# Optimization experiments

Measured on AMD Instinct MI355X. Metric: run time of the kernel, lower is better.

## Reference

```python
import jax, jax.numpy as jnp
import numpy as np

D = 11           # num_classes + 1 (embedding dim)
HL = 7           # window height = 1 + 2*H_PAD
WL = 7           # window width  = 1 + 2*W_PAD
PAD = 3
MAXH, MAXW = 30, 30
FF = 64          # dim_feedforward
EPS = 1e-5       # LayerNorm eps (torch default)
PAD_VALUE = 0.0


def setup_inputs() -> dict:
    key = jax.random.key(0)
    ks = jax.random.split(key, 6)
    N, C, H, W = 1, 10, 16, 16
    s = 0.1
    return {
        "x": jax.random.uniform(ks[0], (N, C, H, W), jnp.float32),
        "Wqkv": jax.random.normal(ks[1], (3 * D, D), jnp.float32) * s,  # in_proj_weight
        "Wo": jax.random.normal(ks[2], (D, D), jnp.float32) * s,        # out_proj.weight
        "W1": jax.random.normal(ks[3], (FF, D), jnp.float32) * s,       # linear1.weight
        "W2": jax.random.normal(ks[4], (D, FF), jnp.float32) * s,       # linear2.weight
        "ln1_w": jnp.ones((D,), jnp.float32),                           # norm1.weight (bias=False)
        "ln2_w": jnp.ones((D,), jnp.float32),                           # norm2.weight (bias=False)
    }


def _layer_norm(x, w):
    m = jnp.mean(x, axis=-1, keepdims=True)
    v = jnp.mean(jnp.square(x - m), axis=-1, keepdims=True)
    return (x - m) / jnp.sqrt(v + EPS) * w


def _encoder_layer(x, Wqkv, Wo, W1, W2, ln1_w, ln2_w):
    # x: [B, S, D]; post-norm, 1 head, no biases, eval mode (dropout off)
    qkv = x @ Wqkv.T
    q, k, v = jnp.split(qkv, 3, axis=-1)
    scale = 1.0 / jnp.sqrt(jnp.float32(D))
    attn = jax.nn.softmax(jnp.einsum('bqd,bkd->bqk', q, k) * scale, axis=-1)
    sa = jnp.einsum('bqk,bkd->bqd', attn, v) @ Wo.T
    x = _layer_norm(x + sa, ln1_w)
    ff = jax.nn.relu(x @ W1.T) @ W2.T
    return _layer_norm(x + ff, ln2_w)


def reference(x, Wqkv, Wo, W1, W2, ln1_w, ln2_w):
    N, C, H, W = x.shape
    C1 = C + 1
    # mask channel: 1 in the padded border, 0 inside
    mask = jnp.pad(jnp.zeros((N, 1, H, W), x.dtype),
                   ((0, 0), (0, 0), (PAD, PAD), (PAD, PAD)), constant_values=1.0)
    xp = jnp.pad(x, ((0, 0), (0, 0), (PAD, PAD), (PAD, PAD)), constant_values=PAD_VALUE)
    xp = jnp.concatenate([xp, mask], axis=1)            # [N, C+1, H+6, W+6]
    win = jnp.stack([xp[:, :, i:i + H, j:j + W]
                     for i in range(HL) for j in range(WL)], axis=-1)  # [N, C1, H, W, 49]
    win = jnp.transpose(win, (0, 2, 3, 1, 4))           # [N, H, W, C1, 49]
    win = win.reshape(N * H * W * C1, HL, WL)
    # embed window into max_height x max_width canvas (rest = pad_value)
    canvas = jnp.full((N * H * W * C1, MAXH, MAXW), PAD_VALUE, x.dtype)
    canvas = canvas.at[:, :HL, :WL].set(win)
    seq = canvas.reshape(N * H * W, C1, MAXH * MAXW).transpose(0, 2, 1)  # [B, S=900, D=11]
    out = _encoder_layer(seq, Wqkv, Wo, W1, W2, ln1_w, ln2_w)
    return out.transpose(0, 2, 1)[:, :-1]               # [B, C, 900]
```

## Files before the change

kernel.cpp:

```cpp
#include <hip/hip_runtime.h>


#define D 11
#define ROWP 12
#define NW 49
#define NWP 52
#define NR 50
#define SEQ 900
#define FFD 64
#define CIN 10
#define NB 256
#define TPB 576
#define NRD (NR * D)

__device__ __forceinline__ float dot12(const float4* a, const float4* b) {
    float4 s = make_float4(0.f, 0.f, 0.f, 0.f);
    #pragma unroll
    for (int i = 0; i < 3; ++i) {
        float4 x = a[i], y = b[i];
        s.x += x.x * y.x; s.y += x.y * y.y; s.z += x.z * y.z; s.w += x.w * y.w;
    }
    return s.x + s.y + s.z + s.w;
}

__global__ __launch_bounds__(TPB) void pve_kernel(
    const float* __restrict__ gx,
    const float* __restrict__ gWqkv,
    const float* __restrict__ gWo,
    const float* __restrict__ gW1,
    const float* __restrict__ gW2,
    const float* __restrict__ gln1,
    const float* __restrict__ gln2,
    float* __restrict__ out)
{
    __shared__ __align__(16) float sQ[33 * ROWP];
    __shared__ __align__(16) float sWo[D * ROWP];
    __shared__ __align__(16) float sW1[FFD * ROWP];
    __shared__ __align__(16) float sW2[D * FFD];
    __shared__ float sln1[D], sln2[D];
    __shared__ __align__(16) float sSeq[NR][ROWP];
    __shared__ __align__(16) float sK[NW][ROWP];
    __shared__ __align__(16) float sVt[D][NWP];
    __shared__ __align__(16) float sQr[NR][ROWP];
    __shared__ __align__(16) float sE[NR][NWP];
    __shared__ __align__(16) float sNum[NR][ROWP];
    __shared__ float sDen[NR];
    __shared__ __align__(16) float sX1[NR][ROWP];
    __shared__ __align__(16) float sX1n[NR][ROWP];
    __shared__ __align__(16) float sH[NR][FFD];
    __shared__ __align__(16) float sY[NR][ROWP];
    __shared__ __align__(16) float sR[NR][ROWP];

    const int tid = threadIdx.x;
    const int b = blockIdx.x;
    const int h = b >> 4;
    const int w = b & 15;

    const int rd = tid;
    const int r = rd / D;
    const int d = rd - r * D;

    for (int i = tid; i < 33 * ROWP; i += TPB) {
        const int rr = i / ROWP, cc = i - rr * ROWP;
        sQ[i] = (cc < D) ? gWqkv[rr * D + cc] : 0.f;
    }
    for (int i = tid; i < D * ROWP; i += TPB) {
        const int rr = i / ROWP, cc = i - rr * ROWP;
        sWo[i] = (cc < D) ? gWo[rr * D + cc] : 0.f;
    }
    for (int i = tid; i < FFD * ROWP; i += TPB) {
        const int rr = i / ROWP, cc = i - rr * ROWP;
        sW1[i] = (cc < D) ? gW1[rr * D + cc] : 0.f;
    }
    for (int i = tid; i < D * FFD; i += TPB) sW2[i] = gW2[i];
    if (tid < D) { sln1[tid] = gln1[tid]; sln2[tid] = gln2[tid]; }

    if (rd < NRD) {
        float val = 0.0f;
        if (r < NW) {
            const int i = r / 7, j = r - (r / 7) * 7;
            const int y = h + i, xx = w + j;
            const bool inter = (y >= 3) && (y < 19) && (xx >= 3) && (xx < 19);
            const int base = inter ? ((y - 3) * 16 + (xx - 3)) : 0;
            if (d < CIN) val = inter ? gx[d * 256 + base] : 0.0f;
            else         val = inter ? 0.0f : 1.0f;
        }
        sSeq[r][d] = val;
        if (d == CIN) sSeq[r][D] = 0.f;
    }
    __syncthreads();

    if (rd < NRD) {
        const float4* sv = (const float4*)&sSeq[r][0];
        const float aq = dot12(sv, (const float4*)&sQ[d * ROWP]);
        const float ak = dot12(sv, (const float4*)&sQ[(D + d) * ROWP]);
        const float av = dot12(sv, (const float4*)&sQ[(2 * D + d) * ROWP]);
        sQr[r][d] = aq;
        if (d == CIN) sQr[r][D] = 0.f;
        if (r < NW) { sK[r][d] = ak; sVt[d][r] = av;
                      if (d == CIN) sK[r][D] = 0.f; }
        else { sVt[d][NW] = 0.f; sVt[d][NW + 1] = 0.f; sVt[d][NW + 2] = 0.f; }
    }
    __syncthreads();

    {
        const float scale = 0.30151134457776363f;
        #pragma unroll
        for (int k = 0; k < 5; ++k) {
            const int idx = tid + k * TPB;
            if (idx < NR * NWP) {
                const int rr = idx / NWP;
                const int tt = idx - rr * NWP;
                float e = 0.f;
                if (tt < NW) {
                    const float s = dot12((const float4*)&sQr[rr][0],
                                          (const float4*)&sK[tt][0]);
                    e = __expf(s * scale);
                }
                sE[rr][tt] = e;
            }
        }
    }
    __syncthreads();

    if (rd < NRD) {
        const float4* ev = (const float4*)&sE[r][0];
        const float4* vv = (const float4*)&sVt[d][0];
        float4 an = make_float4(0.f, 0.f, 0.f, 0.f);
        float4 ad = make_float4(0.f, 0.f, 0.f, 0.f);
        #pragma unroll
        for (int i = 0; i < 13; ++i) {
            const float4 e = ev[i], v = vv[i];
            an.x += e.x * v.x; an.y += e.y * v.y;
            an.z += e.z * v.z; an.w += e.w * v.w;
            ad.x += e.x; ad.y += e.y; ad.z += e.z; ad.w += e.w;
        }
        sNum[r][d] = an.x + an.y + an.z + an.w;
        if (d == CIN) sNum[r][D] = 0.f;
        if (d == 0) sDen[r] = 851.0f + ad.x + ad.y + ad.z + ad.w;
    }
    __syncthreads();

    if (rd < NRD) {
        const float acc = dot12((const float4*)&sNum[r][0],
                                (const float4*)&sWo[d * ROWP]);
        sX1[r][d] = sSeq[r][d] + acc / sDen[r];
        if (d == CIN) sX1[r][D] = 0.f;
    }
    __syncthreads();

    if (rd < NRD) {
        const float4* xv = (const float4*)&sX1[r][0];
        float4 s4 = make_float4(0.f, 0.f, 0.f, 0.f);
        float4 q4 = make_float4(0.f, 0.f, 0.f, 0.f);
        #pragma unroll
        for (int i = 0; i < 3; ++i) {
            const float4 x = xv[i];
            s4.x += x.x; s4.y += x.y; s4.z += x.z; s4.w += x.w;
            q4.x += x.x * x.x; q4.y += x.y * x.y;
            q4.z += x.z * x.z; q4.w += x.w * x.w;
        }
        const float sum = s4.x + s4.y + s4.z + s4.w;
        const float sq  = q4.x + q4.y + q4.z + q4.w;
        const float m   = sum * (1.0f / 11.0f);
        const float var = sq * (1.0f / 11.0f) - m * m;
        sX1n[r][d] = (sX1[r][d] - m) * rsqrtf(var + 1e-5f) * sln1[d];
        if (d == CIN) sX1n[r][D] = 0.f;
    }
    __syncthreads();

    #pragma unroll
    for (int k = 0; k < 6; ++k) {
        const int idx = tid + k * TPB;
        if (idx < NR * FFD) {
            const int rr = idx >> 6;
            const int ff = idx & 63;
            const float acc = dot12((const float4*)&sX1n[rr][0],
                                    (const float4*)&sW1[ff * ROWP]);
            sH[rr][ff] = fmaxf(acc, 0.0f);
        }
    }
    __syncthreads();

    if (rd < NRD) {
        const float4* hv = (const float4*)&sH[r][0];
        const float4* wv = (const float4*)&sW2[d * FFD];
        float4 a4 = make_float4(0.f, 0.f, 0.f, 0.f);
        #pragma unroll
        for (int i = 0; i < 16; ++i) {
            const float4 hh = hv[i], ww = wv[i];
            a4.x += hh.x * ww.x; a4.y += hh.y * ww.y;
            a4.z += hh.z * ww.z; a4.w += hh.w * ww.w;
        }
        sY[r][d] = sX1n[r][d] + a4.x + a4.y + a4.z + a4.w;
        if (d == CIN) sY[r][D] = 0.f;
    }
    __syncthreads();

    if (rd < NRD) {
        const float4* yv = (const float4*)&sY[r][0];
        float4 s4 = make_float4(0.f, 0.f, 0.f, 0.f);
        float4 q4 = make_float4(0.f, 0.f, 0.f, 0.f);
        #pragma unroll
        for (int i = 0; i < 3; ++i) {
            const float4 y = yv[i];
            s4.x += y.x; s4.y += y.y; s4.z += y.z; s4.w += y.w;
            q4.x += y.x * y.x; q4.y += y.y * y.y;
            q4.z += y.z * y.z; q4.w += y.w * y.w;
        }
        const float sum = s4.x + s4.y + s4.z + s4.w;
        const float sq  = q4.x + q4.y + q4.z + q4.w;
        const float m   = sum * (1.0f / 11.0f);
        const float var = sq * (1.0f / 11.0f) - m * m;
        sR[r][d] = (sY[r][d] - m) * rsqrtf(var + 1e-5f) * sln2[d];
    }
    __syncthreads();

    float4* ob4 = (float4*)(out + b * (CIN * SEQ));
    #pragma unroll
    for (int k = 0; k < 4; ++k) {
        const int qi = tid + k * TPB;
        if (qi < 2250) {
            const int c  = qi / 225;
            const int s0 = (qi - c * 225) * 4;
            float4 v4;
            float* pv = (float*)&v4;
            #pragma unroll
            for (int u = 0; u < 4; ++u) {
                const int s = s0 + u;
                const int i = s / 30;
                const int j = s - i * 30;
                pv[u] = (i < 7 && j < 7) ? sR[i * 7 + j][c] : sR[NW][c];
            }
            ob4[qi] = v4;
        }
    }
}

extern "C" void kernel_launch(void* const* d_in, const int* in_sizes, int n_in,
                              void* d_out, int out_size, void* d_ws, size_t ws_size,
                              hipStream_t stream) {
    (void)in_sizes; (void)n_in; (void)out_size; (void)d_ws; (void)ws_size;
    const float* x    = (const float*)d_in[0];
    const float* Wqkv = (const float*)d_in[1];
    const float* Wo   = (const float*)d_in[2];
    const float* W1   = (const float*)d_in[3];
    const float* W2   = (const float*)d_in[4];
    const float* ln1  = (const float*)d_in[5];
    const float* ln2  = (const float*)d_in[6];
    pve_kernel<<<NB, TPB, 0, stream>>>(x, Wqkv, Wo, W1, W2, ln1, ln2,
                                       (float*)d_out);
}
```

Before: 79.80 us.

## Map 16 lanes per row and replace block barriers with wave-local syncs and shuffles

Reassigns threads so each sequence row owns a 16-lane group, with 832 threads per block. This keeps every per-row stage (softmax denominator, attention numerator, both LayerNorms, FFN) inside one wavefront, so several __syncthreads become wave barriers and the row reductions use xor shuffles instead of shared-memory round trips. Several intermediate shared buffers are dropped and the W2 and H rows are padded. The trade-off is more idle lanes (5 of 16 per row) and a larger block, and correctness now depends on each row never crossing a wave boundary.

```diff
diff --git a/kernel.cpp b/kernel.cpp
--- a/kernel.cpp
+++ b/kernel.cpp
@@ -4,14 +4,15 @@
 #define D 11
 #define ROWP 12
 #define NW 49
+#define NR 50
 #define NWP 52
-#define NR 50
+#define FFD 64
+#define W2P 68
+#define HP  68
+#define CIN 10
 #define SEQ 900
-#define FFD 64
-#define CIN 10
 #define NB 256
-#define TPB 576
-#define NRD (NR * D)
+#define TPB 832
 
 __device__ __forceinline__ float dot12(const float4* a, const float4* b) {
     float4 s = make_float4(0.f, 0.f, 0.f, 0.f);
@@ -21,6 +22,12 @@
         s.x += x.x * y.x; s.y += x.y * y.y; s.z += x.z * y.z; s.w += x.w * y.w;
     }
     return s.x + s.y + s.z + s.w;
+}
+
+__device__ __forceinline__ void wave_sync() {
+    __builtin_amdgcn_wave_barrier();
+    asm volatile("s_waitcnt lgkmcnt(0)" ::: "memory");
+    __builtin_amdgcn_wave_barrier();
 }
 
 __global__ __launch_bounds__(TPB) void pve_kernel(
@@ -36,19 +43,15 @@
     __shared__ __align__(16) float sQ[33 * ROWP];
     __shared__ __align__(16) float sWo[D * ROWP];
     __shared__ __align__(16) float sW1[FFD * ROWP];
-    __shared__ __align__(16) float sW2[D * FFD];
-    __shared__ float sln1[D], sln2[D];
+    __shared__ __align__(16) float sW2[D * W2P];
     __shared__ __align__(16) float sSeq[NR][ROWP];
     __shared__ __align__(16) float sK[NW][ROWP];
     __shared__ __align__(16) float sVt[D][NWP];
     __shared__ __align__(16) float sQr[NR][ROWP];
     __shared__ __align__(16) float sE[NR][NWP];
     __shared__ __align__(16) float sNum[NR][ROWP];
-    __shared__ float sDen[NR];
-    __shared__ __align__(16) float sX1[NR][ROWP];
     __shared__ __align__(16) float sX1n[NR][ROWP];
-    __shared__ __align__(16) float sH[NR][FFD];
-    __shared__ __align__(16) float sY[NR][ROWP];
+    __shared__ __align__(16) float sH[NR][HP];
     __shared__ __align__(16) float sR[NR][ROWP];
 
     const int tid = threadIdx.x;
@@ -56,9 +59,10 @@
     const int h = b >> 4;
     const int w = b & 15;
 
-    const int rd = tid;
-    const int r = rd / D;
-    const int d = rd - r * D;
+    const int r = tid >> 4;
+    const int d = tid & 15;
+    const bool rowv = (r < NR);
+    const bool dv = (d < D);
 
     for (int i = tid; i < 33 * ROWP; i += TPB) {
         const int rr = i / ROWP, cc = i - rr * ROWP;
@@ -72,119 +76,140 @@
         const int rr = i / ROWP, cc = i - rr * ROWP;
         sW1[i] = (cc < D) ? gW1[rr * D + cc] : 0.f;
     }
-    for (int i = tid; i < D * FFD; i += TPB) sW2[i] = gW2[i];
-    if (tid < D) { sln1[tid] = gln1[tid]; sln2[tid] = gln2[tid]; }
-
-    if (rd < NRD) {
-        float val = 0.0f;
-        if (r < NW) {
-            const int i = r / 7, j = r - (r / 7) * 7;
-            const int y = h + i, xx = w + j;
-            const bool inter = (y >= 3) && (y < 19) && (xx >= 3) && (xx < 19);
-            const int base = inter ? ((y - 3) * 16 + (xx - 3)) : 0;
-            if (d < CIN) val = inter ? gx[d * 256 + base] : 0.0f;
-            else         val = inter ? 0.0f : 1.0f;
-        }
-        sSeq[r][d] = val;
-        if (d == CIN) sSeq[r][D] = 0.f;
+    for (int i = tid; i < D * W2P; i += TPB) {
+        const int rr = i / W2P, cc = i - rr * W2P;
+        sW2[i] = (cc < FFD) ? gW2[rr * FFD + cc] : 0.f;
+    }
+    float lnw1 = 0.f, lnw2 = 0.f;
+    if (dv) { lnw1 = gln1[d]; lnw2 = gln2[d]; }
+
+    float xin = 0.f;
+    if (rowv) {
+        if (dv) {
+            if (r < NW) {
+                const int i7 = r / 7, j7 = r - i7 * 7;
+                const int y = h + i7, xx = w + j7;
+                const bool inter = (y >= 3) && (y < 19) && (xx >= 3) && (xx < 19);
+                const int base = inter ? ((y - 3) * 16 + (xx - 3)) : 0;
+                if (d < CIN) xin = inter ? gx[d * 256 + base] : 0.0f;
+                else         xin = inter ? 0.0f : 1.0f;
+            }
+            sSeq[r][d] = xin;
+        } else if (d == D) {
+            sSeq[r][D] = 0.f;
+        }
     }
     __syncthreads();
 
-    if (rd < NRD) {
-        const float4* sv = (const float4*)&sSeq[r][0];
-        const float aq = dot12(sv, (const float4*)&sQ[d * ROWP]);
-        const float ak = dot12(sv, (const float4*)&sQ[(D + d) * ROWP]);
-        const float av = dot12(sv, (const float4*)&sQ[(2 * D + d) * ROWP]);
-        sQr[r][d] = aq;
-        if (d == CIN) sQr[r][D] = 0.f;
-        if (r < NW) { sK[r][d] = ak; sVt[d][r] = av;
-                      if (d == CIN) sK[r][D] = 0.f; }
-        else { sVt[d][NW] = 0.f; sVt[d][NW + 1] = 0.f; sVt[d][NW + 2] = 0.f; }
+    if (rowv) {
+        if (dv) {
+            const float4* sv = (const float4*)&sSeq[r][0];
+            const float aq = dot12(sv, (const float4*)&sQ[d * ROWP]);
+            const float ak = dot12(sv, (const float4*)&sQ[(D + d) * ROWP]);
+            const float av = dot12(sv, (const float4*)&sQ[(2 * D + d) * ROWP]);
+            sQr[r][d] = aq;
+            if (r < NW) { sK[r][d] = ak; sVt[d][r] = av; }
+            else { sVt[d][NW] = 0.f; sVt[d][NW + 1] = 0.f; sVt[d][NW + 2] = 0.f; }
+        } else if (d == D) {
+            sQr[r][D] = 0.f;
+            if (r < NW) sK[r][D] = 0.f;
+        }
     }
     __syncthreads();
 
-    {
+    float den = 851.0f;
+    if (rowv) {
         const float scale = 0.30151134457776363f;
+        const float4* qv = (const float4*)&sQr[r][0];
+        const float4 q0 = qv[0], q1 = qv[1], q2 = qv[2];
+        float psum = 0.f;
         #pragma unroll
-        for (int k = 0; k < 5; ++k) {
-            const int idx = tid + k * TPB;
-            if (idx < NR * NWP) {
-                const int rr = idx / NWP;
-                const int tt = idx - rr * NWP;
+        for (int it = 0; it < 4; ++it) {
+            const int tt = d + (it << 4);
+            if (tt < NWP) {
                 float e = 0.f;
                 if (tt < NW) {
-                    const float s = dot12((const float4*)&sQr[rr][0],
-                                          (const float4*)&sK[tt][0]);
+                    const float4* kv = (const float4*)&sK[tt][0];
+                    const float4 k0 = kv[0], k1 = kv[1], k2 = kv[2];
+                    const float s =
+                        q0.x*k0.x + q0.y*k0.y + q0.z*k0.z + q0.w*k0.w +
+                        q1.x*k1.x + q1.y*k1.y + q1.z*k1.z + q1.w*k1.w +
+                        q2.x*k2.x + q2.y*k2.y + q2.z*k2.z + q2.w*k2.w;
                     e = __expf(s * scale);
                 }
-                sE[rr][tt] = e;
-            }
-        }
-    }
-    __syncthreads();
-
-    if (rd < NRD) {
-        const float4* ev = (const float4*)&sE[r][0];
-        const float4* vv = (const float4*)&sVt[d][0];
-        float4 an = make_float4(0.f, 0.f, 0.f, 0.f);
-        float4 ad = make_float4(0.f, 0.f, 0.f, 0.f);
-        #pragma unroll
-        for (int i = 0; i < 13; ++i) {
-            const float4 e = ev[i], v = vv[i];
-            an.x += e.x * v.x; an.y += e.y * v.y;
-            an.z += e.z * v.z; an.w += e.w * v.w;
-            ad.x += e.x; ad.y += e.y; ad.z += e.z; ad.w += e.w;
-        }
-        sNum[r][d] = an.x + an.y + an.z + an.w;
-        if (d == CIN) sNum[r][D] = 0.f;
-        if (d == 0) sDen[r] = 851.0f + ad.x + ad.y + ad.z + ad.w;
-    }
-    __syncthreads();
-
-    if (rd < NRD) {
+                sE[r][tt] = e;
+                psum += e;
+            }
+        }
+        psum += __shfl_xor(psum, 8, 16);
+        psum += __shfl_xor(psum, 4, 16);
+        psum += __shfl_xor(psum, 2, 16);
+        psum += __shfl_xor(psum, 1, 16);
+        den += psum;
+    }
+    wave_sync();
+
+    if (rowv) {
+        if (dv) {
+            const float4* ev = (const float4*)&sE[r][0];
+            const float4* vv = (const float4*)&sVt[d][0];
+            float4 an = make_float4(0.f, 0.f, 0.f, 0.f);
+            #pragma unroll
+            for (int i = 0; i < 13; ++i) {
+                const float4 e = ev[i], v = vv[i];
+                an.x += e.x * v.x; an.y += e.y * v.y;
+                an.z += e.z * v.z; an.w += e.w * v.w;
+            }
+            sNum[r][d] = an.x + an.y + an.z + an.w;
+        } else if (d == D) {
+            sNum[r][D] = 0.f;
+        }
+    }
+    wave_sync();
+
+    float x1 = 0.f;
+    if (rowv && dv) {
         const float acc = dot12((const float4*)&sNum[r][0],
                                 (const float4*)&sWo[d * ROWP]);
-        sX1[r][d] = sSeq[r][d] + acc / sDen[r];
-        if (d == CIN) sX1[r][D] = 0.f;
-    }
-    __syncthreads();
-
-    if (rd < NRD) {
-        const float4* xv = (const float4*)&sX1[r][0];
-        float4 s4 = make_float4(0.f, 0.f, 0.f, 0.f);
-        float4 q4 = make_float4(0.f, 0.f, 0.f, 0.f);
+        x1 = xin + acc / den;
+    }
+    {
+        float s1 = x1, s2 = x1 * x1;
+        s1 += __shfl_xor(s1, 8, 16); s2 += __shfl_xor(s2, 8, 16);
+        s1 += __shfl_xor(s1, 4, 16); s2 += __shfl_xor(s2, 4, 16);
+        s1 += __shfl_xor(s1, 2, 16); s2 += __shfl_xor(s2, 2, 16);
+        s1 += __shfl_xor(s1, 1, 16); s2 += __shfl_xor(s2, 1, 16);
+        const float m   = s1 * (1.0f / 11.0f);
+        const float var = s2 * (1.0f / 11.0f) - m * m;
+        x1 = (x1 - m) * rsqrtf(var + 1e-5f) * lnw1;
+    }
+    if (rowv) {
+        if (dv) sX1n[r][d] = x1;
+        else if (d == D) sX1n[r][D] = 0.f;
+    }
+    wave_sync();
+
+    if (rowv) {
+        const float4* xv = (const float4*)&sX1n[r][0];
+        const float4 xa = xv[0], xb = xv[1], xc = xv[2];
         #pragma unroll
-        for (int i = 0; i < 3; ++i) {
-            const float4 x = xv[i];
-            s4.x += x.x; s4.y += x.y; s4.z += x.z; s4.w += x.w;
-            q4.x += x.x * x.x; q4.y += x.y * x.y;
-            q4.z += x.z * x.z; q4.w += x.w * x.w;
-        }
-        const float sum = s4.x + s4.y + s4.z + s4.w;
-        const float sq  = q4.x + q4.y + q4.z + q4.w;
-        const float m   = sum * (1.0f / 11.0f);
-        const float var = sq * (1.0f / 11.0f) - m * m;
-        sX1n[r][d] = (sX1[r][d] - m) * rsqrtf(var + 1e-5f) * sln1[d];
-        if (d == CIN) sX1n[r][D] = 0.f;
-    }
-    __syncthreads();
-
-    #pragma unroll
-    for (int k = 0; k < 6; ++k) {
-        const int idx = tid + k * TPB;
-        if (idx < NR * FFD) {
-            const int rr = idx >> 6;
-            const int ff = idx & 63;
-            const float acc = dot12((const float4*)&sX1n[rr][0],
-                                    (const float4*)&sW1[ff * ROWP]);
-            sH[rr][ff] = fmaxf(acc, 0.0f);
-        }
-    }
-    __syncthreads();
-
-    if (rd < NRD) {
+        for (int it = 0; it < 4; ++it) {
+            const int ff = d + (it << 4);
+            const float4* wv = (const float4*)&sW1[ff * ROWP];
+            const float4 w0 = wv[0], w1 = wv[1], w2 = wv[2];
+            const float acc =
+                xa.x*w0.x + xa.y*w0.y + xa.z*w0.z + xa.w*w0.w +
+                xb.x*w1.x + xb.y*w1.y + xb.z*w1.z + xb.w*w1.w +
+                xc.x*w2.x + xc.y*w2.y + xc.z*w2.z + xc.w*w2.w;
+            sH[r][ff] = fmaxf(acc, 0.0f);
+        }
+    }
+    wave_sync();
+
+    float yv = 0.f;
+    if (rowv && dv) {
         const float4* hv = (const float4*)&sH[r][0];
-        const float4* wv = (const float4*)&sW2[d * FFD];
+        const float4* wv = (const float4*)&sW2[d * W2P];
         float4 a4 = make_float4(0.f, 0.f, 0.f, 0.f);
         #pragma unroll
         for (int i = 0; i < 16; ++i) {
@@ -192,33 +217,23 @@
             a4.x += hh.x * ww.x; a4.y += hh.y * ww.y;
             a4.z += hh.z * ww.z; a4.w += hh.w * ww.w;
         }
-        sY[r][d] = sX1n[r][d] + a4.x + a4.y + a4.z + a4.w;
-        if (d == CIN) sY[r][D] = 0.f;
-    }
-    __syncthreads();
-
-    if (rd < NRD) {
-        const float4* yv = (const float4*)&sY[r][0];
-        float4 s4 = make_float4(0.f, 0.f, 0.f, 0.f);
-        float4 q4 = make_float4(0.f, 0.f, 0.f, 0.f);
-        #pragma unroll
-        for (int i = 0; i < 3; ++i) {
-            const float4 y = yv[i];
-            s4.x += y.x; s4.y += y.y; s4.z += y.z; s4.w += y.w;
-            q4.x += y.x * y.x; q4.y += y.y * y.y;
-            q4.z += y.z * y.z; q4.w += y.w * y.w;
-        }
-        const float sum = s4.x + s4.y + s4.z + s4.w;
-        const float sq  = q4.x + q4.y + q4.z + q4.w;
-        const float m   = sum * (1.0f / 11.0f);
-        const float var = sq * (1.0f / 11.0f) - m * m;
-        sR[r][d] = (sY[r][d] - m) * rsqrtf(var + 1e-5f) * sln2[d];
+        yv = x1 + a4.x + a4.y + a4.z + a4.w;
+    }
+    {
+        float s1 = yv, s2 = yv * yv;
+        s1 += __shfl_xor(s1, 8, 16); s2 += __shfl_xor(s2, 8, 16);
+        s1 += __shfl_xor(s1, 4, 16); s2 += __shfl_xor(s2, 4, 16);
+        s1 += __shfl_xor(s1, 2, 16); s2 += __shfl_xor(s2, 2, 16);
+        s1 += __shfl_xor(s1, 1, 16); s2 += __shfl_xor(s2, 1, 16);
+        const float m   = s1 * (1.0f / 11.0f);
+        const float var = s2 * (1.0f / 11.0f) - m * m;
+        if (rowv && dv) sR[r][d] = (yv - m) * rsqrtf(var + 1e-5f) * lnw2;
     }
     __syncthreads();
 
     float4* ob4 = (float4*)(out + b * (CIN * SEQ));
     #pragma unroll
-    for (int k = 0; k < 4; ++k) {
+    for (int k = 0; k < 3; ++k) {
         const int qi = tid + k * TPB;
         if (qi < 2250) {
             const int c  = qi / 225;
```

After: 75.00 us. -6.0%, faster.
